# Kernel optimization log

Hardware: AMD Instinct MI355X
Metric: run time of the kernel (lower is better)

Reference implementation:

```python
import jax, jax.numpy as jnp
import numpy as np

EPS_NORM = 1e-12   # F.normalize eps
EPS_PERP = 1e-10   # perplexity log eps
COMMIT = 0.25


def _l2norm(x):
    # matches F.normalize(p=2, dim=1) with eps clamp
    n = jnp.sqrt(jnp.sum(x * x, axis=1, keepdims=True))
    return x / jnp.maximum(n, EPS_NORM)


def setup_inputs() -> dict:
    key = jax.random.key(0)
    k1, k2 = jax.random.split(key)
    B, D, L, K = 8, 256, 4096, 4096
    inputs = jax.random.normal(k1, (B, D, L), dtype=jnp.float32)
    # nn.Embedding init uniform(-1/K, 1/K); use uniform at that scale
    weight = jax.random.uniform(k2, (K, D), minval=-1.0 / K, maxval=1.0 / K, dtype=jnp.float32)
    return {"inputs": inputs, "weight": weight}


def reference(inputs, weight):
    K, D = weight.shape
    x = jnp.transpose(inputs, (0, 2, 1))          # [B, L, D]
    flat = x.reshape(-1, D)                       # [N, D]
    N = flat.shape[0]
    sim = _l2norm(flat) @ _l2norm(weight).T       # [N, K] cosine similarity
    # argmin(1 - sim) == argmax(sim)
    idx = jnp.argmax(sim, axis=1)                 # [N]
    # one-hot @ weight is just a gather of the selected code rows
    quantized = weight[idx].reshape(x.shape)      # [B, L, D]
    e_latent = jnp.mean((jax.lax.stop_gradient(quantized) - x) ** 2)
    q_latent = jnp.mean((quantized - jax.lax.stop_gradient(x)) ** 2)
    loss = q_latent + COMMIT * e_latent
    # straight-through estimator
    q_st = x + jax.lax.stop_gradient(quantized - x)
    # avg_probs = mean of one-hot encodings = normalized histogram of idx
    counts = jnp.zeros((K,), dtype=jnp.float32).at[idx].add(1.0)
    avg_probs = counts / N
    perplexity = jnp.exp(-jnp.sum(avg_probs * jnp.log(avg_probs + EPS_PERP)))
    return jnp.transpose(q_st, (0, 2, 1)), loss, perplexity
```

## Files before the change

### kernel.cpp

```cpp
#include <hip/hip_runtime.h>
#include <stdint.h>

#define Bb 8
#define Dd 256
#define Ll 4096
#define Kk 4096
#define Nn (Bb * Ll)
#define OUT0 (Bb * Dd * Ll)

typedef int    int4v   __attribute__((ext_vector_type(4)));
typedef int    int8v   __attribute__((ext_vector_type(8)));
typedef float  floatx4 __attribute__((ext_vector_type(4)));

#define SCALE1 0x7F7F7F7F

union V8 { int8v v; int4v h[2]; };

__device__ __forceinline__ void async_load16(const void* g, void* l) {
    __builtin_amdgcn_global_load_lds((const __attribute__((address_space(1))) void*)g,
                                     (__attribute__((address_space(3))) void*)l, 16, 0, 0);
}

__global__ void k_prep(const float* __restrict__ w, unsigned char* __restrict__ wn,
                       int* __restrict__ counts) {
    int blk = blockIdx.x, tid = threadIdx.x;
    if (blk == 0)
        for (int i = tid; i < Kk + 2; i += 256) counts[i] = 0;
    int row  = blk * 4 + (tid >> 6);
    int lane = tid & 63;
    float4 v = ((const float4*)(w + (size_t)row * Dd))[lane];
    float ss = v.x*v.x + v.y*v.y + v.z*v.z + v.w*v.w;
#pragma unroll
    for (int m = 1; m < 64; m <<= 1) ss += __shfl_xor(ss, m, 64);
    float s = 16.0f / fmaxf(sqrtf(ss), 1e-12f);
    int p = __builtin_amdgcn_cvt_pk_fp8_f32(v.x * s, v.y * s, 0, false);
    p     = __builtin_amdgcn_cvt_pk_fp8_f32(v.z * s, v.w * s, p, true);
    ((int*)(wn + (size_t)row * Dd))[lane] = p;
}

__global__ __launch_bounds__(256, 2) void k_gemm_fused(
        const float* __restrict__ x, const unsigned char* __restrict__ Wn,
        const float* __restrict__ w, float* __restrict__ out,
        int* __restrict__ counts) {
    __shared__ __align__(16) unsigned char As[64 * 256];
    __shared__ __align__(16) unsigned char Bs[4][3][16 * 256];
    __shared__ unsigned int red[64][4];
    __shared__ int kidx[64];
    __shared__ float wsum[4];
    __shared__ int lastp;

    float* lossacc = (float*)(counts + Kk);
    int*   done    = counts + Kk + 1;

    int bid = blockIdx.x;
    int bm = ((bid & 7) << 6) | (bid >> 3);
    int tid = threadIdx.x, lane = tid & 63, wv = tid >> 6;
    int l15 = lane & 15, l4 = lane >> 4;

    int goff[4], loff[4];
#pragma unroll
    for (int j = 0; j < 4; ++j) {
        int c = j * 4 + l4;
        goff[j] = c * 256 + ((l15 ^ (c & 15)) << 4);
        loff[j] = j * 1024 + lane * 16;
    }

#pragma unroll
    for (int j = 0; j < 4; ++j)
        async_load16(Wn + (size_t)(0 * 4 + wv) * 4096 + goff[j],
                     Bs[wv][0] + loff[j]);
#pragma unroll
    for (int j = 0; j < 4; ++j)
        async_load16(Wn + (size_t)(1 * 4 + wv) * 4096 + goff[j],
                     Bs[wv][1] + loff[j]);

    int b = bm >> 6, l0 = (bm & 63) * 64;
    const float* xs = x + (size_t)b * Dd * Ll + l0;
    int lg = tid & 15, dgr = tid >> 4;
#pragma unroll
    for (int i = 0; i < 4; ++i) {
        int d0 = dgr * 4 + i * 64;
        const float* s0 = xs + (size_t)d0 * Ll + lg * 4;
        float4 f0 = *(const float4*)(s0);
        float4 f1 = *(const float4*)(s0 + Ll);
        float4 f2 = *(const float4*)(s0 + 2 * (size_t)Ll);
        float4 f3 = *(const float4*)(s0 + 3 * (size_t)Ll);
#pragma unroll
        for (int jl = 0; jl < 4; ++jl) {
            float a0 = ((const float*)&f0)[jl], a1 = ((const float*)&f1)[jl];
            float a2 = ((const float*)&f2)[jl], a3 = ((const float*)&f3)[jl];
            int pk = __builtin_amdgcn_cvt_pk_fp8_f32(a0, a1, 0, false);
            pk     = __builtin_amdgcn_cvt_pk_fp8_f32(a2, a3, pk, true);
            int l = lg * 4 + jl;
            *(int*)(As + l * 256 + (((d0 >> 4) ^ (l & 15)) << 4) + (d0 & 15)) = pk;
        }
    }
    __syncthreads();

    int8v af[4][2];
#pragma unroll
    for (int fm = 0; fm < 4; ++fm)
#pragma unroll
        for (int ks = 0; ks < 2; ++ks) {
            int l = fm * 16 + l15;
            int ch = ks * 8 + l4 * 2;
            V8 u;
            u.h[0] = *(const int4v*)(As + l * 256 + ((ch ^ l15) << 4));
            u.h[1] = *(const int4v*)(As + l * 256 + (((ch + 1) ^ l15) << 4));
            af[fm][ks] = u.v;
        }

    unsigned int rk[4][4];
#pragma unroll
    for (int fm = 0; fm < 4; ++fm)
#pragma unroll
        for (int r = 0; r < 4; ++r) rk[fm][r] = 0u;

    int base0 = l15 * 256;
    for (int t = 0; t < 64; ++t) {
        const unsigned char* p0 = Bs[wv][t % 3];
        unsigned char*       p2 = Bs[wv][(t + 2) % 3];
        if (t == 63) asm volatile("s_waitcnt vmcnt(0)" ::: "memory");
        else         asm volatile("s_waitcnt vmcnt(4)" ::: "memory");
        __builtin_amdgcn_sched_barrier(0);
        if (t < 62) {
            const unsigned char* g = Wn + (size_t)((t + 2) * 4 + wv) * 4096;
#pragma unroll
            for (int j = 0; j < 4; ++j)
                async_load16(g + goff[j], p2 + loff[j]);
        }
        V8 bf0, bf1;
        bf0.h[0] = *(const int4v*)(p0 + base0 + (((l4 * 2 + 0) ^ l15) << 4));
        bf0.h[1] = *(const int4v*)(p0 + base0 + (((l4 * 2 + 1) ^ l15) << 4));
        bf1.h[0] = *(const int4v*)(p0 + base0 + (((8 + l4 * 2 + 0) ^ l15) << 4));
        bf1.h[1] = *(const int4v*)(p0 + base0 + (((8 + l4 * 2 + 1) ^ l15) << 4));
        __builtin_amdgcn_s_setprio(1);
        floatx4 acc[4];
#pragma unroll
        for (int fm = 0; fm < 4; ++fm) {
            floatx4 a = (floatx4)512.0f;
            a = __builtin_amdgcn_mfma_scale_f32_16x16x128_f8f6f4(
                    af[fm][0], bf0.v, a, 0, 0, 0, SCALE1, 0, SCALE1);
            a = __builtin_amdgcn_mfma_scale_f32_16x16x128_f8f6f4(
                    af[fm][1], bf1.v, a, 0, 0, 0, SCALE1, 0, SCALE1);
            acc[fm] = a;
        }
        __builtin_amdgcn_s_setprio(0);
        unsigned int i0 = (unsigned)((t * 4 + wv) * 16 + l15);
#pragma unroll
        for (int fm = 0; fm < 4; ++fm)
#pragma unroll
            for (int r = 0; r < 4; ++r) {
                unsigned int k0 = (__float_as_uint(acc[fm][r]) & 0xFFFFF000u) | i0;
                rk[fm][r] = rk[fm][r] > k0 ? rk[fm][r] : k0;
            }
    }

#pragma unroll
    for (int fm = 0; fm < 4; ++fm)
#pragma unroll
        for (int r = 0; r < 4; ++r) {
            unsigned int kx = rk[fm][r];
#pragma unroll
            for (int md = 1; md <= 8; md <<= 1) {
                unsigned int o = (unsigned int)__shfl_xor((int)kx, md, 64);
                kx = kx > o ? kx : o;
            }
            if (l15 == 0) red[fm * 16 + l4 * 4 + r][wv] = kx;
        }
    __syncthreads();
    if (tid < 64) {
        unsigned int k0 = red[tid][0], k1 = red[tid][1];
        unsigned int k2 = red[tid][2], k3 = red[tid][3];
        unsigned int kx = k0 > k1 ? k0 : k1;
        kx = kx > k2 ? kx : k2;
        kx = kx > k3 ? kx : k3;
        int ix = (int)(kx & 0xFFFu);
        kidx[tid] = ix;
        atomicAdd(&counts[ix], 1);
    }
    __syncthreads();

    float ls = 0.f;
    {
        float* os = out + (size_t)b * Dd * Ll + l0;
        int r0 = lg * 4;
#pragma unroll
        for (int i = 0; i < 4; ++i) {
            int d0 = dgr * 4 + i * 64;
            float4 xv[4];
#pragma unroll
            for (int dd = 0; dd < 4; ++dd)
                xv[dd] = *(const float4*)(xs + (size_t)(d0 + dd) * Ll + lg * 4);
            float4 q4[4];
#pragma unroll
            for (int jl = 0; jl < 4; ++jl)
                q4[jl] = *(const float4*)(w + (size_t)kidx[r0 + jl] * Dd + d0);
#pragma unroll
            for (int dd = 0; dd < 4; ++dd) {
                float4 qq;
                qq.x = ((const float*)&q4[0])[dd];
                qq.y = ((const float*)&q4[1])[dd];
                qq.z = ((const float*)&q4[2])[dd];
                qq.w = ((const float*)&q4[3])[dd];
                float e0 = qq.x - xv[dd].x, e1 = qq.y - xv[dd].y;
                float e2 = qq.z - xv[dd].z, e3 = qq.w - xv[dd].w;
                ls += e0*e0 + e1*e1 + e2*e2 + e3*e3;
                *(float4*)(os + (size_t)(d0 + dd) * Ll + lg * 4) = qq;
            }
        }
    }

#pragma unroll
    for (int m = 1; m < 64; m <<= 1) ls += __shfl_xor(ls, m, 64);
    if (lane == 0) wsum[wv] = ls;
    __syncthreads();
    if (tid == 0) {
        atomicAdd(lossacc, wsum[0] + wsum[1] + wsum[2] + wsum[3]);
        __threadfence();
        lastp = (atomicAdd(done, 1) == 511);
    }
    __syncthreads();
    if (lastp) {
        __threadfence();
        float s = 0.f;
        for (int i = tid; i < Kk; i += 256) {
            float p = (float)counts[i] * (1.0f / Nn);
            s += p * logf(p + 1e-10f);
        }
#pragma unroll
        for (int m = 1; m < 64; m <<= 1) s += __shfl_xor(s, m, 64);
        if (lane == 0) wsum[wv] = s;
        __syncthreads();
        if (tid == 0) {
            out[OUT0]     = lossacc[0] * 1.25f / (float)OUT0;
            out[OUT0 + 1] = expf(-(wsum[0] + wsum[1] + wsum[2] + wsum[3]));
        }
    }
}

extern "C" void kernel_launch(void* const* d_in, const int* in_sizes, int n_in,
                              void* d_out, int out_size, void* d_ws, size_t ws_size,
                              hipStream_t stream) {
    const float* x = (const float*)d_in[0];
    const float* w = (const float*)d_in[1];
    float* out = (float*)d_out;
    char* ws = (char*)d_ws;

    unsigned char* wn     = (unsigned char*)ws;
    int*           counts = (int*)(ws + (1u << 20));

    k_prep      <<<1024, 256, 0, stream>>>(w, wn, counts);
    k_gemm_fused<<<512,  256, 0, stream>>>(x, wn, w, out, counts);
}
```

Baseline: 168.5 us.

## Split gather epilogue into separate kernel and prefetch B fragments one step ahead

Moves the gather, straight-through output write and loss accumulation out of the GEMM kernel into a new 1024-block epilogue kernel that reads the argmax indices from a workspace buffer. The GEMM main loop now register-prefetches the next LDS B fragment before issuing the MFMAs, and it waits on vmcnt(0) each iteration instead of vmcnt(4). The goal is to hide LDS read latency and to spread the memory-bound epilogue over more blocks. In exchange it adds a third kernel launch and a round trip of the indices through global memory, and the stricter wait may expose global-load latency in the loop.

```diff
diff --git a/kernel.cpp b/kernel.cpp
--- a/kernel.cpp
+++ b/kernel.cpp
@@ -38,19 +38,12 @@
     ((int*)(wn + (size_t)row * Dd))[lane] = p;
 }
 
-__global__ __launch_bounds__(256, 2) void k_gemm_fused(
+__global__ __launch_bounds__(256, 2) void k_gemm(
         const float* __restrict__ x, const unsigned char* __restrict__ Wn,
-        const float* __restrict__ w, float* __restrict__ out,
-        int* __restrict__ counts) {
+        int* __restrict__ idxout, int* __restrict__ counts) {
     __shared__ __align__(16) unsigned char As[64 * 256];
     __shared__ __align__(16) unsigned char Bs[4][3][16 * 256];
     __shared__ unsigned int red[64][4];
-    __shared__ int kidx[64];
-    __shared__ float wsum[4];
-    __shared__ int lastp;
-
-    float* lossacc = (float*)(counts + Kk);
-    int*   done    = counts + Kk + 1;
 
     int bid = blockIdx.x;
     int bm = ((bid & 7) << 6) | (bid >> 3);
@@ -117,32 +110,38 @@
         for (int r = 0; r < 4; ++r) rk[fm][r] = 0u;
 
     int base0 = l15 * 256;
+#define DSRD(D0, D1, P)                                                       \
+    do {                                                                      \
+        const unsigned char* pp_ = (P);                                       \
+        D0.h[0] = *(const int4v*)(pp_ + base0 + (((l4 * 2 + 0) ^ l15) << 4)); \
+        D0.h[1] = *(const int4v*)(pp_ + base0 + (((l4 * 2 + 1) ^ l15) << 4)); \
+        D1.h[0] = *(const int4v*)(pp_ + base0 + (((8 + l4 * 2) ^ l15) << 4)); \
+        D1.h[1] = *(const int4v*)(pp_ + base0 + (((9 + l4 * 2) ^ l15) << 4)); \
+    } while (0)
+
+    V8 bfA0, bfA1, bfB0, bfB1;
+    DSRD(bfA0, bfA1, Bs[wv][0]);
+
+#pragma unroll 2
     for (int t = 0; t < 64; ++t) {
-        const unsigned char* p0 = Bs[wv][t % 3];
-        unsigned char*       p2 = Bs[wv][(t + 2) % 3];
-        if (t == 63) asm volatile("s_waitcnt vmcnt(0)" ::: "memory");
-        else         asm volatile("s_waitcnt vmcnt(4)" ::: "memory");
-        __builtin_amdgcn_sched_barrier(0);
+        asm volatile("s_waitcnt vmcnt(0)" ::: "memory");
         if (t < 62) {
             const unsigned char* g = Wn + (size_t)((t + 2) * 4 + wv) * 4096;
+            unsigned char* lb = Bs[wv][(t + 2) % 3];
 #pragma unroll
             for (int j = 0; j < 4; ++j)
-                async_load16(g + goff[j], p2 + loff[j]);
-        }
-        V8 bf0, bf1;
-        bf0.h[0] = *(const int4v*)(p0 + base0 + (((l4 * 2 + 0) ^ l15) << 4));
-        bf0.h[1] = *(const int4v*)(p0 + base0 + (((l4 * 2 + 1) ^ l15) << 4));
-        bf1.h[0] = *(const int4v*)(p0 + base0 + (((8 + l4 * 2 + 0) ^ l15) << 4));
-        bf1.h[1] = *(const int4v*)(p0 + base0 + (((8 + l4 * 2 + 1) ^ l15) << 4));
+                async_load16(g + goff[j], lb + loff[j]);
+        }
+        if (t < 63) DSRD(bfB0, bfB1, Bs[wv][(t + 1) % 3]);
         __builtin_amdgcn_s_setprio(1);
         floatx4 acc[4];
 #pragma unroll
         for (int fm = 0; fm < 4; ++fm) {
             floatx4 a = (floatx4)512.0f;
             a = __builtin_amdgcn_mfma_scale_f32_16x16x128_f8f6f4(
-                    af[fm][0], bf0.v, a, 0, 0, 0, SCALE1, 0, SCALE1);
+                    af[fm][0], bfA0.v, a, 0, 0, 0, SCALE1, 0, SCALE1);
             a = __builtin_amdgcn_mfma_scale_f32_16x16x128_f8f6f4(
-                    af[fm][1], bf1.v, a, 0, 0, 0, SCALE1, 0, SCALE1);
+                    af[fm][1], bfA1.v, a, 0, 0, 0, SCALE1, 0, SCALE1);
             acc[fm] = a;
         }
         __builtin_amdgcn_s_setprio(0);
@@ -154,7 +153,9 @@
                 unsigned int k0 = (__float_as_uint(acc[fm][r]) & 0xFFFFF000u) | i0;
                 rk[fm][r] = rk[fm][r] > k0 ? rk[fm][r] : k0;
             }
-    }
+        bfA0 = bfB0; bfA1 = bfB1;
+    }
+#undef DSRD
 
 #pragma unroll
     for (int fm = 0; fm < 4; ++fm)
@@ -176,39 +177,57 @@
         kx = kx > k2 ? kx : k2;
         kx = kx > k3 ? kx : k3;
         int ix = (int)(kx & 0xFFFu);
-        kidx[tid] = ix;
+        idxout[bm * 64 + tid] = ix;
         atomicAdd(&counts[ix], 1);
     }
-    __syncthreads();
-
+}
+
+__global__ __launch_bounds__(256) void k_epi(
+        const float* __restrict__ x, const float* __restrict__ w,
+        const int* __restrict__ idx, float* __restrict__ out,
+        int* __restrict__ counts) {
+    __shared__ int kidx[32];
+    __shared__ float wsum[4];
+    __shared__ int lastp;
+
+    float* lossacc = (float*)(counts + Kk);
+    int*   done    = counts + Kk + 1;
+
+    int bid = blockIdx.x;
+    int bm = ((bid & 7) << 7) | (bid >> 3);
+    int tid = threadIdx.x, lane = tid & 63, wv = tid >> 6;
+    int b = bm >> 7, l0 = (bm & 127) * 32;
+    if (tid < 32) kidx[tid] = idx[bm * 32 + tid];
+    __syncthreads();
+
+    int lg = tid & 7, dgr = tid >> 3;
+    const float* xs = x + (size_t)b * Dd * Ll + l0;
+    float*       os = out + (size_t)b * Dd * Ll + l0;
+    int r0 = lg * 4, d0 = dgr * 8;
+
+    float4 xv[8], q4[4][2];
+#pragma unroll
+    for (int dd = 0; dd < 8; ++dd)
+        xv[dd] = *(const float4*)(xs + (size_t)(d0 + dd) * Ll + lg * 4);
+#pragma unroll
+    for (int jl = 0; jl < 4; ++jl) {
+        const float* wr = w + (size_t)kidx[r0 + jl] * Dd + d0;
+        q4[jl][0] = *(const float4*)(wr);
+        q4[jl][1] = *(const float4*)(wr + 4);
+    }
     float ls = 0.f;
-    {
-        float* os = out + (size_t)b * Dd * Ll + l0;
-        int r0 = lg * 4;
-#pragma unroll
-        for (int i = 0; i < 4; ++i) {
-            int d0 = dgr * 4 + i * 64;
-            float4 xv[4];
-#pragma unroll
-            for (int dd = 0; dd < 4; ++dd)
-                xv[dd] = *(const float4*)(xs + (size_t)(d0 + dd) * Ll + lg * 4);
-            float4 q4[4];
-#pragma unroll
-            for (int jl = 0; jl < 4; ++jl)
-                q4[jl] = *(const float4*)(w + (size_t)kidx[r0 + jl] * Dd + d0);
-#pragma unroll
-            for (int dd = 0; dd < 4; ++dd) {
-                float4 qq;
-                qq.x = ((const float*)&q4[0])[dd];
-                qq.y = ((const float*)&q4[1])[dd];
-                qq.z = ((const float*)&q4[2])[dd];
-                qq.w = ((const float*)&q4[3])[dd];
-                float e0 = qq.x - xv[dd].x, e1 = qq.y - xv[dd].y;
-                float e2 = qq.z - xv[dd].z, e3 = qq.w - xv[dd].w;
-                ls += e0*e0 + e1*e1 + e2*e2 + e3*e3;
-                *(float4*)(os + (size_t)(d0 + dd) * Ll + lg * 4) = qq;
-            }
-        }
+#pragma unroll
+    for (int dd = 0; dd < 8; ++dd) {
+        int h = dd >> 2, c = dd & 3;
+        float4 qq;
+        qq.x = ((const float*)&q4[0][h])[c];
+        qq.y = ((const float*)&q4[1][h])[c];
+        qq.z = ((const float*)&q4[2][h])[c];
+        qq.w = ((const float*)&q4[3][h])[c];
+        float e0 = qq.x - xv[dd].x, e1 = qq.y - xv[dd].y;
+        float e2 = qq.z - xv[dd].z, e3 = qq.w - xv[dd].w;
+        ls += e0*e0 + e1*e1 + e2*e2 + e3*e3;
+        *(float4*)(os + (size_t)(d0 + dd) * Ll + lg * 4) = qq;
     }
 
 #pragma unroll
@@ -218,7 +237,7 @@
     if (tid == 0) {
         atomicAdd(lossacc, wsum[0] + wsum[1] + wsum[2] + wsum[3]);
         __threadfence();
-        lastp = (atomicAdd(done, 1) == 511);
+        lastp = (atomicAdd(done, 1) == 1023);
     }
     __syncthreads();
     if (lastp) {
@@ -249,7 +268,9 @@
 
     unsigned char* wn     = (unsigned char*)ws;
     int*           counts = (int*)(ws + (1u << 20));
-
-    k_prep      <<<1024, 256, 0, stream>>>(w, wn, counts);
-    k_gemm_fused<<<512,  256, 0, stream>>>(x, wn, w, out, counts);
-}
+    int*           idxb   = (int*)(ws + (1u << 20) + (32u << 10));
+
+    k_prep<<<1024, 256, 0, stream>>>(w, wn, counts);
+    k_gemm<<<512,  256, 0, stream>>>(x, wn, idxb, counts);
+    k_epi <<<1024, 256, 0, stream>>>(x, w, idxb, out, counts);
+}
```

Result: slower. 190.8 us (+13.3%).
